# Kernel optimization log

Measured on AMD Instinct MI355X. Metric: run time of the kernel, lower is better.

## Reference

```python
import jax, jax.numpy as jnp
import numpy as np
import math

B, NQ, D = 2, 5000, 256
HEADS, LVLS, PTS, NREF = 8, 4, 8, 4  # PTS = all_sampling_points, NREF = ref points per query
DH = D // HEADS
SHAPES = [(100, 100), (50, 50), (25, 25), (13, 13)]
NV = sum(h * w for h, w in SHAPES)


def _grid_init_bias():
    # replicates DeformableSatAttention.init_weights sampling_offsets bias
    thetas = np.arange(HEADS, dtype=np.float32) * (2.0 * math.pi / HEADS)
    grid = np.stack([np.cos(thetas), np.sin(thetas)], -1)
    grid = grid / np.abs(grid).max(-1, keepdims=True)
    grid = np.tile(grid.reshape(HEADS, 1, 1, 2), (1, LVLS, PTS, 1))  # PTS == HEADS
    for i in range(PTS):
        grid[:, :, i, :] *= i + 1
    return jnp.asarray(grid.reshape(-1), dtype=jnp.float32)


def setup_inputs() -> dict:
    key = jax.random.key(0)
    ks = jax.random.split(key, 8)
    xb = math.sqrt(6.0 / (D + D))  # xavier uniform bound for value_proj
    return {
        "query": jax.random.normal(ks[0], (B, NQ, D), jnp.float32),
        "key": jax.random.normal(ks[1], (B, NV, D), jnp.float32),
        "value": jax.random.normal(ks[2], (B, NV, D), jnp.float32),
        "reference_points": jax.random.uniform(ks[3], (B, NQ, NREF, 2), jnp.float32),
        "spatial_shapes": jnp.asarray(SHAPES, jnp.int32),
        "level_start_index": jnp.asarray(np.cumsum([0] + [h * w for h, w in SHAPES])[:-1], jnp.int32),
        "W_value": jax.random.uniform(ks[4], (D, D), jnp.float32, -xb, xb),
        "b_value": jnp.zeros((D,), jnp.float32),
        "W_offset": 0.01 * jax.random.normal(ks[5], (D, HEADS * LVLS * PTS * 2), jnp.float32),
        "b_offset": _grid_init_bias(),
        "W_attn": 0.01 * jax.random.normal(ks[6], (D, HEADS * LVLS * PTS), jnp.float32),
        "b_attn": jnp.zeros((HEADS * LVLS * PTS,), jnp.float32),
    }


def _bilinear(vflat, H, W, loc):
    # vflat: [B, H*W, HEADS, DH]; loc: [B, NQ, HEADS, PTS, 2] in [0,1]
    # grid_sample-style align_corners=False, zero padding (as in MSDeformAttn CUDA)
    x = loc[..., 0] * W - 0.5
    y = loc[..., 1] * H - 0.5
    x0 = jnp.floor(x)
    y0 = jnp.floor(y)
    dx = x - x0
    dy = y - y0
    x0i = x0.astype(jnp.int32)
    y0i = y0.astype(jnp.int32)

    def gather(ix, iy):
        valid = ((ix >= 0) & (ix < W) & (iy >= 0) & (iy < H)).astype(vflat.dtype)
        idx = jnp.clip(iy, 0, H - 1) * W + jnp.clip(ix, 0, W - 1)  # [B,NQ,HEADS,PTS]
        b, nq, h, p = idx.shape
        idx2 = idx.transpose(0, 1, 3, 2).reshape(b, nq * p, h)
        g = jnp.take_along_axis(vflat, idx2[..., None], axis=1)  # [B,NQ*PTS,HEADS,DH]
        g = g.reshape(b, nq, p, h, -1).transpose(0, 1, 3, 2, 4)  # [B,NQ,HEADS,PTS,DH]
        return g * valid[..., None]

    g00 = gather(x0i, y0i)
    g01 = gather(x0i + 1, y0i)
    g10 = gather(x0i, y0i + 1)
    g11 = gather(x0i + 1, y0i + 1)
    w00 = ((1 - dx) * (1 - dy))[..., None]
    w01 = (dx * (1 - dy))[..., None]
    w10 = ((1 - dx) * dy)[..., None]
    w11 = (dx * dy)[..., None]
    return g00 * w00 + g01 * w01 + g10 * w10 + g11 * w11


def reference(query, key, value, reference_points, spatial_shapes, level_start_index,
              W_value, b_value, W_offset, b_offset, W_attn, b_attn):
    bs, nq, _ = query.shape
    v = (value @ W_value + b_value).reshape(bs, -1, HEADS, DH)
    off = (query @ W_offset + b_offset).reshape(bs, nq, HEADS, LVLS, PTS, 2)
    aw = jax.nn.softmax((query @ W_attn + b_attn).reshape(bs, nq, HEADS, LVLS * PTS), axis=-1)
    aw = aw.reshape(bs, nq, HEADS, LVLS, PTS)
    shapes = np.asarray(spatial_shapes)  # static level geometry
    starts = np.asarray(level_start_index)
    # offset_normalizer = (W, H) per level
    norm = jnp.asarray(np.stack([shapes[:, 1], shapes[:, 0]], -1), jnp.float32)
    off = off / norm[None, None, None, :, None, :]
    off = off.reshape(bs, nq, HEADS, LVLS, PTS // NREF, NREF, 2)
    loc = reference_points[:, :, None, None, None, :, :] + off
    loc = loc.reshape(bs, nq, HEADS, LVLS, PTS, 2)
    out = jnp.zeros((bs, nq, HEADS, DH), v.dtype)
    for l in range(shapes.shape[0]):
        Hl, Wl = int(shapes[l, 0]), int(shapes[l, 1])
        s = int(starts[l])
        vl = v[:, s:s + Hl * Wl]
        sampled = _bilinear(vl, Hl, Wl, loc[:, :, :, l])  # [B,NQ,HEADS,PTS,DH]
        out = out + (sampled * aw[:, :, :, l][..., None]).sum(axis=3)
    return out.reshape(bs, nq, D)
```

## Files before the change

kernel.cpp:

```cpp
#include <hip/hip_runtime.h>
#include <math.h>

#define HEADS 8
#define LVLS  4
#define PTS   8
#define NREF  4
#define DH    32
#define DD    256
#define NQc   5000
#define BATCH 2
#define NVc   13294
#define RVr   (BATCH * NVc)
#define RQr   (BATCH * NQc)

#define NJV 832
#define NJQ 942
#define NJOBS (NJV + NJQ)

using f16x8 = __attribute__((ext_vector_type(8))) _Float16;
using f16x4 = __attribute__((ext_vector_type(4))) _Float16;
using f32x4 = __attribute__((ext_vector_type(4))) float;
using h2    = __attribute__((ext_vector_type(2))) _Float16;

__device__ __forceinline__ int pack2(float w) {
    _Float16 h = (_Float16)w;
    h2 v = { h, h };
    return __builtin_bit_cast(int, v);
}

__global__ __launch_bounds__(256) void transpose_w_kernel(
    const float* __restrict__ Wv, const float* __restrict__ Wo,
    const float* __restrict__ Wa,
    _Float16* __restrict__ wtv, _Float16* __restrict__ wto,
    _Float16* __restrict__ wta)
{
    __shared__ float tl[64][65];
    const int bid = blockIdx.x;
    const float* src; _Float16* dst; int N, kt, nt;
    if (bid < 16)      { src = Wv; dst = wtv; N = 256; kt = bid & 3;        nt = bid >> 2; }
    else if (bid < 48) { src = Wo; dst = wto; N = 512; kt = (bid - 16) & 3; nt = (bid - 16) >> 2; }
    else               { src = Wa; dst = wta; N = 256; kt = (bid - 48) & 3; nt = (bid - 48) >> 2; }
    const int k0 = kt * 64, n0 = nt * 64;
    const int c  = threadIdx.x & 63, r4 = threadIdx.x >> 6;
    #pragma unroll
    for (int i = 0; i < 16; ++i) {
        const int r = r4 + i * 4;
        tl[r][c] = src[(size_t)(k0 + r) * N + n0 + c];
    }
    __syncthreads();
    #pragma unroll
    for (int i = 0; i < 16; ++i) {
        const int r = r4 + i * 4;
        dst[(size_t)(n0 + r) * 256 + k0 + c] = (_Float16)tl[c][r];
    }
}

__global__ __launch_bounds__(256) void gemm_uber_kernel(
    const float* __restrict__ value, const float* __restrict__ query,
    const _Float16* __restrict__ wtv, const _Float16* __restrict__ wtoa,
    const float* __restrict__ bv, const float* __restrict__ bo,
    const float* __restrict__ ba,
    _Float16* __restrict__ v_f16, _Float16* __restrict__ offa)
{
    __shared__ _Float16 aL[64][72];
    __shared__ _Float16 bL[128][64];

    const int t    = threadIdx.x;
    const int lane = t & 63;
    const int wid  = t >> 6;
    const int wr   = wid >> 1;
    const int wc   = wid & 1;

    const int job = blockIdx.x;
    const bool isV = job < NJV;
    const float* A; const _Float16* WT; int R, r0, ct;
    if (isV) { A = value; WT = wtv;  R = RVr; r0 = (job >> 1) * 64;  ct = job & 1; }
    else     { const int j2 = job - NJV;
               A = query; WT = wtoa; R = RQr; r0 = (j2 / 6) * 64;    ct = j2 % 6; }
    const int c0 = ct * 128;

    f32x4 acc[2][4] = {};

    const int sr = t >> 4;
    const int sc = (t & 15) * 4;
    const int brow  = lane >> 3;
    const int bslot = (lane & 7) ^ brow;

    for (int kc = 0; kc < 256; kc += 64) {
        __syncthreads();
        #pragma unroll
        for (int cch = 0; cch < 4; ++cch) {
            const int ch  = wid * 4 + cch;
            const int row = ch * 8 + brow;
            const _Float16* src = WT + (size_t)(c0 + row) * 256 + kc + bslot * 8;
            char* ldst = (char*)&bL[0][0] + ch * 1024;
            __builtin_amdgcn_global_load_lds(
                (const __attribute__((address_space(1))) void*)src,
                (__attribute__((address_space(3))) void*)ldst, 16, 0, 0);
        }
        #pragma unroll
        for (int i = 0; i < 4; ++i) {
            const int row = sr + i * 16;
            const int gr  = r0 + row;
            float4 vv = make_float4(0.f, 0.f, 0.f, 0.f);
            if (gr < R) vv = *(const float4*)&A[(size_t)gr * 256 + kc + sc];
            f16x4 pk = { (_Float16)vv.x, (_Float16)vv.y, (_Float16)vv.z, (_Float16)vv.w };
            *(f16x4*)&aL[row][sc] = pk;
        }
        __syncthreads();

        const int lm  = lane & 15;
        const int khi = lane >> 4;
        const char* bB = (const char*)&bL[0][0];
        #pragma unroll
        for (int kk = 0; kk < 2; ++kk) {
            f16x8 bfrag[4];
            #pragma unroll
            for (int nf = 0; nf < 4; ++nf) {
                const int row  = wc * 64 + nf * 16 + lm;
                const int slot = kk * 4 + khi;
                bfrag[nf] = *(const f16x8*)(bB + row * 128 + ((slot ^ (row & 7)) << 4));
            }
            #pragma unroll
            for (int m = 0; m < 2; ++m) {
                const f16x8 afrag = *(const f16x8*)&aL[wr * 32 + m * 16 + lm][kk * 32 + khi * 8];
                #pragma unroll
                for (int nf = 0; nf < 4; ++nf)
                    acc[m][nf] = __builtin_amdgcn_mfma_f32_16x16x32_f16(
                        afrag, bfrag[nf], acc[m][nf], 0, 0, 0);
            }
        }
    }

    const int lm = lane & 15;
    const int lq = lane >> 4;
    if (isV) {
        #pragma unroll
        for (int nf = 0; nf < 4; ++nf) {
            const int col = c0 + wc * 64 + nf * 16 + lm;
            const int hh = col >> 5, ch = col & 31;
            const float bb = bv[col];
            #pragma unroll
            for (int m = 0; m < 2; ++m)
                #pragma unroll
                for (int r = 0; r < 4; ++r) {
                    const int row = r0 + wr * 32 + m * 16 + lq * 4 + r;
                    if (row < RVr) {
                        const int b   = (row >= NVc) ? 1 : 0;
                        const int pix = row - b * NVc;
                        v_f16[(((size_t)(b * HEADS + hh) * NVc) + pix) * 32 + ch] =
                            (_Float16)(acc[m][nf][r] + bb);
                    }
                }
        }
    } else {
        #pragma unroll
        for (int nf = 0; nf < 4; ++nf) {
            const int col = c0 + wc * 64 + nf * 16 + lm;
            const float bb = (col < 512) ? bo[col] : ba[col - 512];
            #pragma unroll
            for (int m = 0; m < 2; ++m)
                #pragma unroll
                for (int r = 0; r < 4; ++r) {
                    const int row = r0 + wr * 32 + m * 16 + lq * 4 + r;
                    if (row < RQr) offa[(size_t)row * 768 + col] = (_Float16)(acc[m][nf][r] + bb);
                }
        }
    }
}

__global__ __launch_bounds__(256) void sample_kernel(
    const _Float16* __restrict__ v,
    const _Float16* __restrict__ offa,
    const float* __restrict__ refp,
    float* __restrict__ out)
{
    __shared__ int2 swa[4][32][5];

    const int t    = threadIdx.x;
    const int wv   = t >> 6;
    const int lane = t & 63;
    const int j    = lane & 31;
    const int half = lane >> 5;

    const int task = blockIdx.x * 4 + wv;
    const int h  = task & 7;
    const int bq = task >> 3;
    const int b  = bq / NQc;

    {
        const int l = j >> 3;
        const int p = j & 7;
        const int r = p & 3;
        const int   Wi = (l == 0) ? 100 : (l == 1) ? 50 : (l == 2) ? 25 : 13;
        const float Wf = (float)Wi;
        const int   st = (l == 0) ? 0 : (l == 1) ? 10000 : (l == 2) ? 12500 : 13125;

        const _Float16* orow = offa + (size_t)bq * 768;
        const float lg = (float)orow[512 + h * 32 + j];
        const float e  = __expf(lg);
        float s = e;
        #pragma unroll
        for (int mask = 16; mask >= 1; mask >>= 1)
            s += __shfl_xor(s, mask, 64);
        const float aw = __fdividef(e, s);

        const h2 oxy = *(const h2*)&orow[h * 64 + j * 2];
        const float2 rxy = *(const float2*)&refp[((size_t)bq * NREF + r) * 2];

        const float x = rxy.x * Wf + (float)oxy[0] - 0.5f;
        const float y = rxy.y * Wf + (float)oxy[1] - 0.5f;
        const float x0f = floorf(x), y0f = floorf(y);
        const float dx = x - x0f, dy = y - y0f;
        const int x0 = (int)x0f, y0 = (int)y0f;
        const int x1 = x0 + 1;

        const int   yy = y0 + half;
        const float fy = (half ? dy : 1.f - dy) * aw;
        const bool  vy = (yy >= 0) && (yy < Wi);
        const int   yc = min(max(yy, 0), Wi - 1);

        const bool vx0 = (x0 >= 0) && (x0 < Wi);
        const bool vx1 = (x1 >= 0) && (x1 < Wi);
        const int  xc0 = min(max(x0, 0), Wi - 1);
        const int  xc1 = min(max(x1, 0), Wi - 1);

        const int bb   = ((b * HEADS + h) * NVc + st) * 64;
        const int rowb = bb + yc * Wi * 64;
        const float wA = (vx0 && vy) ? (1.f - dx) * fy : 0.f;
        const float wB = (vx1 && vy) ? dx * fy : 0.f;

        swa[wv][j][half * 2 + 0] = make_int2(rowb + (xc0 << 6), pack2(wA));
        swa[wv][j][half * 2 + 1] = make_int2(rowb + (xc1 << 6), pack2(wB));
    }

    const int po  = lane >> 4;
    const int c   = (lane >> 2) & 3;
    const int cqb = (lane & 3) * 16;

    h2 acc0 = {}, acc1 = {}, acc2 = {}, acc3 = {};
    #pragma unroll
    for (int it = 0; it < 8; ++it) {
        const int2 aw2 = swa[wv][it * 4 + po][c];
        const h2 w2 = __builtin_bit_cast(h2, aw2.y);
        const f16x8 val = *(const f16x8*)((const char*)v + aw2.x + cqb);
        acc0 += w2 * (h2){ val[0], val[1] };
        acc1 += w2 * (h2){ val[2], val[3] };
        acc2 += w2 * (h2){ val[4], val[5] };
        acc3 += w2 * (h2){ val[6], val[7] };
    }

    #pragma unroll
    for (int mask = 4; mask <= 32; mask <<= 1) {
        acc0 += __builtin_bit_cast(h2, __shfl_xor(__builtin_bit_cast(int, acc0), mask, 64));
        acc1 += __builtin_bit_cast(h2, __shfl_xor(__builtin_bit_cast(int, acc1), mask, 64));
        acc2 += __builtin_bit_cast(h2, __shfl_xor(__builtin_bit_cast(int, acc2), mask, 64));
        acc3 += __builtin_bit_cast(h2, __shfl_xor(__builtin_bit_cast(int, acc3), mask, 64));
    }

    if (lane < 4) {
        float* dst = &out[(size_t)bq * 256 + h * 32 + lane * 8];
        *(float4*)(dst + 0) = make_float4((float)acc0[0], (float)acc0[1],
                                          (float)acc1[0], (float)acc1[1]);
        *(float4*)(dst + 4) = make_float4((float)acc2[0], (float)acc2[1],
                                          (float)acc3[0], (float)acc3[1]);
    }
}

extern "C" void kernel_launch(void* const* d_in, const int* in_sizes, int n_in,
                              void* d_out, int out_size, void* d_ws, size_t ws_size,
                              hipStream_t stream)
{
    const float* query  = (const float*)d_in[0];
    const float* value  = (const float*)d_in[2];
    const float* refp   = (const float*)d_in[3];
    const float* Wv     = (const float*)d_in[6];
    const float* bv     = (const float*)d_in[7];
    const float* Wo     = (const float*)d_in[8];
    const float* bo     = (const float*)d_in[9];
    const float* Wa     = (const float*)d_in[10];
    const float* ba     = (const float*)d_in[11];
    float* out = (float*)d_out;

    _Float16* v_f16 = (_Float16*)d_ws;
    _Float16* offa  = v_f16 + (size_t)RVr * 256;
    _Float16* wtv   = offa + (size_t)RQr * 768;
    _Float16* wtoa  = wtv + 256 * 256;

    transpose_w_kernel<<<dim3(64), 256, 0, stream>>>(
        Wv, Wo, Wa, wtv, wtoa, wtoa + 512 * 256);

    gemm_uber_kernel<<<dim3(NJOBS), 256, 0, stream>>>(
        value, query, wtv, wtoa, bv, bo, ba, v_f16, offa);

    sample_kernel<<<dim3(RQr * HEADS / 4), 256, 0, stream>>>(
        v_f16, offa, refp, out);
}
```

Baseline: 81.31 us.

## Double-buffer GEMM K-loop and enlarge row tile to 128 in uber kernel

The fused value/query projection GEMM now processes 128-row tiles instead of 64, halving the job count, and double-buffers both the A and B tiles in shared memory. Global loads for the next K chunk are issued into registers and LDS before the MFMAs on the current chunk, and the converted A tile is stored afterwards, so memory latency overlaps compute. This doubles accumulator registers and LDS use, which may lower occupancy, and leaves fewer blocks to spread across the GPU.

```diff
diff --git a/kernel.cpp b/kernel.cpp
--- a/kernel.cpp
+++ b/kernel.cpp
@@ -13,8 +13,8 @@
 #define RVr   (BATCH * NVc)
 #define RQr   (BATCH * NQc)
 
-#define NJV 832
-#define NJQ 942
+#define NJV 416
+#define NJQ 474
 #define NJOBS (NJV + NJQ)
 
 using f16x8 = __attribute__((ext_vector_type(8))) _Float16;
@@ -62,8 +62,8 @@
     const float* __restrict__ ba,
     _Float16* __restrict__ v_f16, _Float16* __restrict__ offa)
 {
-    __shared__ _Float16 aL[64][72];
-    __shared__ _Float16 bL[128][64];
+    __shared__ _Float16 aL[2][128][72];
+    __shared__ _Float16 bL[2][128][64];
 
     const int t    = threadIdx.x;
     const int lane = t & 63;
@@ -74,44 +74,70 @@
     const int job = blockIdx.x;
     const bool isV = job < NJV;
     const float* A; const _Float16* WT; int R, r0, ct;
-    if (isV) { A = value; WT = wtv;  R = RVr; r0 = (job >> 1) * 64;  ct = job & 1; }
+    if (isV) { A = value; WT = wtv;  R = RVr; r0 = (job >> 1) * 128;  ct = job & 1; }
     else     { const int j2 = job - NJV;
-               A = query; WT = wtoa; R = RQr; r0 = (j2 / 6) * 64;    ct = j2 % 6; }
+               A = query; WT = wtoa; R = RQr; r0 = (j2 / 6) * 128;    ct = j2 % 6; }
     const int c0 = ct * 128;
 
-    f32x4 acc[2][4] = {};
+    f32x4 acc[4][4] = {};
 
     const int sr = t >> 4;
     const int sc = (t & 15) * 4;
     const int brow  = lane >> 3;
     const int bslot = (lane & 7) ^ brow;
-
-    for (int kc = 0; kc < 256; kc += 64) {
-        __syncthreads();
-        #pragma unroll
-        for (int cch = 0; cch < 4; ++cch) {
-            const int ch  = wid * 4 + cch;
-            const int row = ch * 8 + brow;
-            const _Float16* src = WT + (size_t)(c0 + row) * 256 + kc + bslot * 8;
-            char* ldst = (char*)&bL[0][0] + ch * 1024;
-            __builtin_amdgcn_global_load_lds(
-                (const __attribute__((address_space(1))) void*)src,
-                (__attribute__((address_space(3))) void*)ldst, 16, 0, 0);
-        }
-        #pragma unroll
-        for (int i = 0; i < 4; ++i) {
-            const int row = sr + i * 16;
-            const int gr  = r0 + row;
-            float4 vv = make_float4(0.f, 0.f, 0.f, 0.f);
-            if (gr < R) vv = *(const float4*)&A[(size_t)gr * 256 + kc + sc];
-            f16x4 pk = { (_Float16)vv.x, (_Float16)vv.y, (_Float16)vv.z, (_Float16)vv.w };
-            *(f16x4*)&aL[row][sc] = pk;
-        }
-        __syncthreads();
-
-        const int lm  = lane & 15;
-        const int khi = lane >> 4;
-        const char* bB = (const char*)&bL[0][0];
+    const int lm  = lane & 15;
+    const int khi = lane >> 4;
+
+    float4 ap[8];
+
+    #pragma unroll
+    for (int cch = 0; cch < 4; ++cch) {
+        const int ch  = wid * 4 + cch;
+        const int row = ch * 8 + brow;
+        const _Float16* src = WT + (size_t)(c0 + row) * 256 + 0 + bslot * 8;
+        char* ldst = (char*)&bL[0][0][0] + ch * 1024;
+        __builtin_amdgcn_global_load_lds(
+            (const __attribute__((address_space(1))) void*)src,
+            (__attribute__((address_space(3))) void*)ldst, 16, 0, 0);
+    }
+    #pragma unroll
+    for (int i = 0; i < 8; ++i) {
+        const int gr = r0 + sr + i * 16;
+        ap[i] = (gr < R) ? *(const float4*)&A[(size_t)gr * 256 + sc]
+                         : make_float4(0.f, 0.f, 0.f, 0.f);
+    }
+    #pragma unroll
+    for (int i = 0; i < 8; ++i) {
+        f16x4 pk = { (_Float16)ap[i].x, (_Float16)ap[i].y,
+                     (_Float16)ap[i].z, (_Float16)ap[i].w };
+        *(f16x4*)&aL[0][sr + i * 16][sc] = pk;
+    }
+    __syncthreads();
+
+    #pragma unroll
+    for (int tk = 0; tk < 4; ++tk) {
+        const int cur = tk & 1;
+        if (tk < 3) {
+            const int kc = (tk + 1) * 64;
+            #pragma unroll
+            for (int cch = 0; cch < 4; ++cch) {
+                const int ch  = wid * 4 + cch;
+                const int row = ch * 8 + brow;
+                const _Float16* src = WT + (size_t)(c0 + row) * 256 + kc + bslot * 8;
+                char* ldst = (char*)&bL[cur ^ 1][0][0] + ch * 1024;
+                __builtin_amdgcn_global_load_lds(
+                    (const __attribute__((address_space(1))) void*)src,
+                    (__attribute__((address_space(3))) void*)ldst, 16, 0, 0);
+            }
+            #pragma unroll
+            for (int i = 0; i < 8; ++i) {
+                const int gr = r0 + sr + i * 16;
+                ap[i] = (gr < R) ? *(const float4*)&A[(size_t)gr * 256 + kc + sc]
+                                 : make_float4(0.f, 0.f, 0.f, 0.f);
+            }
+        }
+
+        const char* bB = (const char*)&bL[cur][0][0];
         #pragma unroll
         for (int kk = 0; kk < 2; ++kk) {
             f16x8 bfrag[4];
@@ -122,17 +148,26 @@
                 bfrag[nf] = *(const f16x8*)(bB + row * 128 + ((slot ^ (row & 7)) << 4));
             }
             #pragma unroll
-            for (int m = 0; m < 2; ++m) {
-                const f16x8 afrag = *(const f16x8*)&aL[wr * 32 + m * 16 + lm][kk * 32 + khi * 8];
+            for (int m = 0; m < 4; ++m) {
+                const f16x8 afrag = *(const f16x8*)&aL[cur][wr * 64 + m * 16 + lm][kk * 32 + khi * 8];
                 #pragma unroll
                 for (int nf = 0; nf < 4; ++nf)
                     acc[m][nf] = __builtin_amdgcn_mfma_f32_16x16x32_f16(
                         afrag, bfrag[nf], acc[m][nf], 0, 0, 0);
             }
         }
-    }
-
-    const int lm = lane & 15;
+
+        if (tk < 3) {
+            #pragma unroll
+            for (int i = 0; i < 8; ++i) {
+                f16x4 pk = { (_Float16)ap[i].x, (_Float16)ap[i].y,
+                             (_Float16)ap[i].z, (_Float16)ap[i].w };
+                *(f16x4*)&aL[cur ^ 1][sr + i * 16][sc] = pk;
+            }
+        }
+        __syncthreads();
+    }
+
     const int lq = lane >> 4;
     if (isV) {
         #pragma unroll
@@ -141,10 +176,10 @@
             const int hh = col >> 5, ch = col & 31;
             const float bb = bv[col];
             #pragma unroll
-            for (int m = 0; m < 2; ++m)
+            for (int m = 0; m < 4; ++m)
                 #pragma unroll
                 for (int r = 0; r < 4; ++r) {
-                    const int row = r0 + wr * 32 + m * 16 + lq * 4 + r;
+                    const int row = r0 + wr * 64 + m * 16 + lq * 4 + r;
                     if (row < RVr) {
                         const int b   = (row >= NVc) ? 1 : 0;
                         const int pix = row - b * NVc;
@@ -159,10 +194,10 @@
             const int col = c0 + wc * 64 + nf * 16 + lm;
             const float bb = (col < 512) ? bo[col] : ba[col - 512];
             #pragma unroll
-            for (int m = 0; m < 2; ++m)
+            for (int m = 0; m < 4; ++m)
                 #pragma unroll
                 for (int r = 0; r < 4; ++r) {
-                    const int row = r0 + wr * 32 + m * 16 + lq * 4 + r;
+                    const int row = r0 + wr * 64 + m * 16 + lq * 4 + r;
                     if (row < RQr) offa[(size_t)row * 768 + col] = (_Float16)(acc[m][nf][r] + bb);
                 }
         }
```

After: 98.28 us. 1.21x slower.
